# Performance work log

Measured on AMD Instinct MI355X. Metric: run time of the kernel, lower is better.

## Reference

```python
import jax, jax.numpy as jnp
import numpy as np
from jax import lax

EPS = 1e-5


def _up2_align_corners(x):
    # UpsamplingBilinear2d(scale_factor=2) => align_corners=True
    B, C, H, W = x.shape
    def idx(n):
        pos = jnp.arange(2 * n, dtype=jnp.float32) * ((n - 1) / (2 * n - 1))
        i0 = jnp.floor(pos).astype(jnp.int32)
        i1 = jnp.minimum(i0 + 1, n - 1)
        f = (pos - i0).astype(x.dtype)
        return i0, i1, f
    i0, i1, f = idx(H)
    x = x[:, :, i0, :] * (1 - f)[None, None, :, None] + x[:, :, i1, :] * f[None, None, :, None]
    j0, j1, g = idx(W)
    x = x[:, :, :, j0] * (1 - g) + x[:, :, :, j1] * g
    return x


def _forward(x, w_off, b_off, w_dcn, b_dcn, gamma, beta, run_mean, run_var):
    B, C, H, W = x.shape
    Cout = w_dcn.shape[0]
    # conv_offset: 27 = deform_groups*3*3*3 channels -> (o1, o2, mask)
    om = lax.conv_general_dilated(x, w_off, (1, 1), ((1, 1), (1, 1)),
                                  dimension_numbers=('NCHW', 'OIHW', 'NCHW'))
    om = om + b_off[None, :, None, None]
    o1, o2, m = om[:, :9], om[:, 9:18], om[:, 18:]
    off = jnp.concatenate([o1, o2], axis=1)          # [B,18,H,W]
    dy = off[:, 0::2]                                 # [B,9,H,W] per-kernel-point dy
    dx = off[:, 1::2]                                 # [B,9,H,W] per-kernel-point dx
    mask = jax.nn.sigmoid(m)                          # [B,9,H,W]
    # sampling positions: p + p_k + offset, stride=1, pad=1, dilation=1
    ky = jnp.array([-1, -1, -1, 0, 0, 0, 1, 1, 1], jnp.float32)
    kx = jnp.array([-1, 0, 1, -1, 0, 1, -1, 0, 1], jnp.float32)
    py = dy + jnp.arange(H, dtype=jnp.float32)[None, None, :, None] + ky[None, :, None, None]
    px = dx + jnp.arange(W, dtype=jnp.float32)[None, None, None, :] + kx[None, :, None, None]
    y0 = jnp.floor(py); x0 = jnp.floor(px)
    fy = py - y0; fx = px - x0
    y0i = y0.astype(jnp.int32); x0i = x0.astype(jnp.int32)
    xf = x.reshape(B, C, H * W)
    KHW = 9 * H * W
    def gather(yi, xi, wgt):
        valid = ((yi >= 0) & (yi < H) & (xi >= 0) & (xi < W)).astype(x.dtype)
        idx = jnp.clip(yi, 0, H - 1) * W + jnp.clip(xi, 0, W - 1)
        g = jnp.take_along_axis(xf, jnp.broadcast_to(idx.reshape(B, 1, KHW), (B, C, KHW)), axis=2)
        return g.reshape(B, C, 9, H, W) * (wgt * valid)[:, None]
    s = (gather(y0i, x0i, (1 - fy) * (1 - fx))
         + gather(y0i, x0i + 1, (1 - fy) * fx)
         + gather(y0i + 1, x0i, fy * (1 - fx))
         + gather(y0i + 1, x0i + 1, fy * fx))
    s = s * mask[:, None]                             # modulated sampling
    out = jnp.einsum('bckhw,ock->bohw', s, w_dcn.reshape(Cout, C, 9))
    out = out + b_dcn[None, :, None, None]
    # BatchNorm (eval mode with running stats) + ReLU
    scale = (gamma * lax.rsqrt(run_var + EPS))[None, :, None, None]
    out = out * scale + (beta - gamma * run_mean * lax.rsqrt(run_var + EPS))[None, :, None, None]
    out = jax.nn.relu(out)
    return _up2_align_corners(out)


def setup_inputs() -> dict:
    key = jax.random.key(0)
    ks = jax.random.split(key, 9)
    B, Cin, H, W, Cout = 4, 256, 64, 64, 128
    x = jax.random.normal(ks[0], (B, Cin, H, W), jnp.float32)
    w_off = jax.random.normal(ks[1], (27, Cin, 3, 3), jnp.float32) * 0.01
    b_off = jax.random.normal(ks[2], (27,), jnp.float32) * 0.1
    w_dcn = jax.random.normal(ks[3], (Cout, Cin, 3, 3), jnp.float32) * 0.05
    b_dcn = jax.random.normal(ks[4], (Cout,), jnp.float32) * 0.01
    gamma = 1.0 + 0.1 * jax.random.normal(ks[5], (Cout,), jnp.float32)
    beta = 0.1 * jax.random.normal(ks[6], (Cout,), jnp.float32)
    run_mean = 0.1 * jax.random.normal(ks[7], (Cout,), jnp.float32)
    run_var = jax.random.uniform(ks[8], (Cout,), jnp.float32) + 0.5
    return {"x": x, "w_off": w_off, "b_off": b_off, "w_dcn": w_dcn, "b_dcn": b_dcn,
            "gamma": gamma, "beta": beta, "run_mean": run_mean, "run_var": run_var}


def reference(x, w_off, b_off, w_dcn, b_dcn, gamma, beta, run_mean, run_var):
    return _forward(x, w_off, b_off, w_dcn, b_dcn, gamma, beta, run_mean, run_var)
```

## Files before the change

### kernel.cpp

```cpp
#include <hip/hip_runtime.h>
#include <math.h>

#define CIN  256
#define COUT 128
#define HW   4096
#define NB   4
#define OCSPLIT 4
#define CSPLIT  2
#define CPC  (CIN / CSPLIT)
#define SFLAV (576 * 16)

typedef short short8v __attribute__((ext_vector_type(8)));
typedef float f32x4  __attribute__((ext_vector_type(4)));

__global__ __launch_bounds__(256) void k_prep_w(
    const float* __restrict__ w_dcn, const float* __restrict__ b_dcn,
    const float* __restrict__ gamma, const float* __restrict__ beta,
    const float* __restrict__ rmean, const float* __restrict__ rvar,
    unsigned short* __restrict__ w_hi, unsigned short* __restrict__ w_lo,
    float* __restrict__ bias_t)
{
  int t = blockIdx.x * 256 + threadIdx.x;
  if (t < COUT) {
    float sc = gamma[t] * rsqrtf(rvar[t] + 1e-5f);
    bias_t[t] = b_dcn[t] * sc + beta[t] - rmean[t] * sc;
  }
  if (t >= CIN * COUT * 9) return;
  int k = t % 9;
  int q = t / 9;
  int co = q % COUT;
  int c  = q / COUT;
  float sc = gamma[co] * rsqrtf(rvar[co] + 1e-5f);
  float w = w_dcn[((size_t)co * CIN + c) * 9 + k] * sc;
  unsigned int wb = __float_as_uint(w);
  unsigned short hi = (unsigned short)(wb >> 16);
  float lof = w - __uint_as_float(wb & 0xFFFF0000u);
  unsigned short lo = (unsigned short)(__float_as_uint(lof) >> 16);
  size_t idx = (((size_t)k * 32 + (c >> 3)) * 128 + co) * 8 + (c & 7);
  w_hi[idx] = hi;
  w_lo[idx] = lo;
}

__global__ __launch_bounds__(256) void k_prep_wo(
    const float* __restrict__ w_off,
    unsigned short* __restrict__ wo_hi, unsigned short* __restrict__ wo_lo)
{
  int t = blockIdx.x * 256 + threadIdx.x;
  if (t >= 9 * 32 * 32 * 8) return;
  int ce = t & 7;
  int co = (t >> 3) & 31;
  int cq = (t >> 8) & 31;
  int k  = t >> 13;
  int c = cq * 8 + ce;
  float w = (co < 27) ? w_off[((size_t)co * CIN + c) * 9 + k] : 0.f;
  unsigned int wb = __float_as_uint(w);
  unsigned short hi = (unsigned short)(wb >> 16);
  float lof = w - __uint_as_float(wb & 0xFFFF0000u);
  unsigned short lo = (unsigned short)(__float_as_uint(lof) >> 16);
  wo_hi[t] = hi;
  wo_lo[t] = lo;
}

__global__ __launch_bounds__(256, 4) void k_off_mfma(
    const float* __restrict__ x,
    const unsigned short* __restrict__ wo_hi, const unsigned short* __restrict__ wo_lo,
    float* __restrict__ om_part)
{
  int blk = (blockIdx.x & 7) * 128 + (blockIdx.x >> 3);
  int split = blk & 3;
  int bh = blk >> 2;
  int b = bh >> 6, h = bh & 63;
  int t = threadIdx.x;
  int lane = t & 63;
  int wv = t >> 6;
  int lrow = lane & 15, lgrp = lane >> 4;

  __shared__ __align__(16) unsigned int win_hi[3 * 66 * 20];
  __shared__ __align__(16) unsigned int win_lo[3 * 66 * 20];

  f32x4 acc[2];
  acc[0] = (f32x4){0.f, 0.f, 0.f, 0.f};
  acc[1] = (f32x4){0.f, 0.f, 0.f, 0.f};

  const float* xb = x + (size_t)b * CIN * HW;

  for (int chunk = 0; chunk < 2; ++chunk) {
    int cbase = split * 64 + chunk * 32;
    for (int i = t; i < 3168; i += 256) {
      int cp = i / 198;
      int s  = i - cp * 198;
      int r  = s / 66;
      int colp = s - r * 66;
      int row = h + r - 1;
      int col = colp - 1;
      bool v = ((unsigned)row < 64u) && ((unsigned)col < 64u);
      int ch = cbase + 2 * cp;
      float f0 = 0.f, f1 = 0.f;
      if (v) {
        const float* xp = xb + ((size_t)ch * 64 + row) * 64 + col;
        f0 = xp[0];
        f1 = xp[HW];
      }
      unsigned a0 = __float_as_uint(f0), a1 = __float_as_uint(f1);
      unsigned hi = (a0 >> 16) | (a1 & 0xFFFF0000u);
      float l0 = f0 - __uint_as_float(a0 & 0xFFFF0000u);
      float l1 = f1 - __uint_as_float(a1 & 0xFFFF0000u);
      unsigned lo = (__float_as_uint(l0) >> 16) | (__float_as_uint(l1) & 0xFFFF0000u);
      win_hi[s * 20 + cp] = hi;
      win_lo[s * 20 + cp] = lo;
    }
    __syncthreads();

    int pos = wv * 16 + lrow;
#pragma unroll
    for (int k = 0; k < 9; ++k) {
      int ky = k / 3 - 1, kx = k % 3 - 1;
      int slot = (ky + 1) * 66 + pos + kx + 1;
      const unsigned int* ph = &win_hi[slot * 20 + lgrp * 4];
      const unsigned int* pl = &win_lo[slot * 20 + lgrp * 4];
      short8v bh = *(const short8v*)ph;
      short8v bl = *(const short8v*)pl;
#pragma unroll
      for (int m = 0; m < 2; ++m) {
        size_t widx = (((size_t)k * 32 + (cbase >> 3) + lgrp) * 32 + m * 16 + lrow) * 8;
        short8v ah = *(const short8v*)(wo_hi + widx);
        short8v al = *(const short8v*)(wo_lo + widx);
        acc[m] = __builtin_amdgcn_mfma_f32_16x16x32_bf16(ah, bh, acc[m], 0, 0, 0);
        acc[m] = __builtin_amdgcn_mfma_f32_16x16x32_bf16(ah, bl, acc[m], 0, 0, 0);
        acc[m] = __builtin_amdgcn_mfma_f32_16x16x32_bf16(al, bh, acc[m], 0, 0, 0);
      }
    }
    __syncthreads();
  }

  int pos = wv * 16 + lrow;
#pragma unroll
  for (int m = 0; m < 2; ++m)
#pragma unroll
    for (int j = 0; j < 4; ++j) {
      int co = m * 16 + lgrp * 4 + j;
      if (co < 27)
        om_part[(((size_t)split * NB + b) * 27 + co) * HW + h * 64 + pos] = acc[m][j];
    }
}

__global__ __launch_bounds__(256) void k_prep_md(
    const float* __restrict__ om_part, const float* __restrict__ b_off,
    float4* __restrict__ md_w, int4* __restrict__ md_i)
{
  int t = blockIdx.x * 256 + threadIdx.x;
  if (t >= NB * 9 * HW) return;
  int hw = t & 4095;
  int bk = t >> 12;
  int k = bk % 9;
  int b = bk / 9;
  int h = hw >> 6, w = hw & 63;

  float dy = b_off[2 * k], dx = b_off[2 * k + 1], mr = b_off[18 + k];
#pragma unroll
  for (int s = 0; s < OCSPLIT; ++s) {
    size_t o = ((size_t)s * NB + b) * 27 * HW + hw;
    dy += om_part[o + (size_t)(2 * k) * HW];
    dx += om_part[o + (size_t)(2 * k + 1) * HW];
    mr += om_part[o + (size_t)(18 + k) * HW];
  }
  float m = 1.0f / (1.0f + expf(-mr));

  int ky = k / 3 - 1, kx = k % 3 - 1;
  float py = dy + (float)h + (float)ky;
  float px = dx + (float)w + (float)kx;
  float y0f = floorf(py), x0f = floorf(px);
  float fy = py - y0f, fx = px - x0f;
  int y0 = (int)y0f, x0 = (int)x0f;
  int y1 = y0 + 1, x1 = x0 + 1;

  bool vy0 = (y0 >= 0) & (y0 < 64), vy1 = (y1 >= 0) & (y1 < 64);
  bool vx0 = (x0 >= 0) & (x0 < 64), vx1 = (x1 >= 0) & (x1 < 64);
  int cy0 = min(max(y0, 0), 63), cy1 = min(max(y1, 0), 63);
  int cx0 = min(max(x0, 0), 63), cx1 = min(max(x1, 0), 63);

  float4 wv;
  wv.x = (vy0 && vx0) ? (1.f - fy) * (1.f - fx) * m : 0.f;
  wv.y = (vy0 && vx1) ? (1.f - fy) * fx * m : 0.f;
  wv.z = (vy1 && vx0) ? fy * (1.f - fx) * m : 0.f;
  wv.w = (vy1 && vx1) ? fy * fx * m : 0.f;
  int4 iv;
  iv.x = cy0 * 64 + cx0;
  iv.y = cy0 * 64 + cx1;
  iv.z = cy1 * 64 + cx0;
  iv.w = cy1 * 64 + cx1;
  md_w[t] = wv;
  md_i[t] = iv;
}

__global__ __launch_bounds__(256, 3) void k_dcn(
    const float* __restrict__ x,
    const unsigned short* __restrict__ w_hi, const unsigned short* __restrict__ w_lo,
    const float4* __restrict__ md_w, const int4* __restrict__ md_i,
    float* __restrict__ part)
{
  int blk = (blockIdx.x & 7) * 64 + (blockIdx.x >> 3);
  int h = blk & 63;
  int b = (blk >> 6) & (NB - 1);
  int s2 = blk >> 8;
  int c0 = s2 * CPC;
  int t = threadIdx.x;
  int lane = t & 63;
  int wv = t >> 6;
  int lrow = lane & 15, lgrp = lane >> 4;

  __shared__ __align__(16) unsigned int sbuf[SFLAV];
  __shared__ __align__(16) float win[8 * 64 * 4];

  int W0 = min(max(h - 3, 0), 56);
  int ob = W0 * 64;

  int k0 = t >> 6;
  size_t mdbase = (size_t)b * 9 * HW;
  size_t mdp = mdbase + (size_t)h * 64 + (t & 63);
  float4 mw0 = md_w[mdp + (size_t)k0 * HW];
  int4  mi0 = md_i[mdp + (size_t)k0 * HW];
  float4 mw1 = md_w[mdp + (size_t)(k0 + 4) * HW];
  int4  mi1 = md_i[mdp + (size_t)(k0 + 4) * HW];
  bool hasC = (t < 64);
  float4 mw2 = make_float4(0.f, 0.f, 0.f, 0.f);
  int4  mi2 = make_int4(0, 0, 0, 0);
  if (hasC) {
    mw2 = md_w[mdp + (size_t)8 * HW];
    mi2 = md_i[mdp + (size_t)8 * HW];
  }
  int fast0 = __all(((unsigned)(mi0.x - ob) < 512u) && ((unsigned)(mi0.z - ob) < 512u));
  int fast1 = __all(((unsigned)(mi1.x - ob) < 512u) && ((unsigned)(mi1.z - ob) < 512u));
  int fast2 = __all(((unsigned)(mi2.x - ob) < 512u) && ((unsigned)(mi2.z - ob) < 512u));

  f32x4 acc[2][4];
#pragma unroll
  for (int m = 0; m < 2; ++m)
#pragma unroll
    for (int nt = 0; nt < 4; ++nt)
      acc[m][nt] = (f32x4){0.f, 0.f, 0.f, 0.f};

  const float* xb = x + (size_t)b * CIN * HW;

#define GATHER(MW, MI, FASTE, ROW)                                              \
  {                                                                             \
    float s0_, s1_, s2_, s3_;                                                   \
    if (FASTE) {                                                                \
      float4 T0 = *(const float4*)&win[(MI.x - ob) * 4];                        \
      float4 T1 = *(const float4*)&win[(MI.y - ob) * 4];                        \
      float4 T2 = *(const float4*)&win[(MI.z - ob) * 4];                        \
      float4 T3 = *(const float4*)&win[(MI.w - ob) * 4];                        \
      s0_ = MW.x * T0.x + MW.y * T1.x + MW.z * T2.x + MW.w * T3.x;              \
      s1_ = MW.x * T0.y + MW.y * T1.y + MW.z * T2.y + MW.w * T3.y;              \
      s2_ = MW.x * T0.z + MW.y * T1.z + MW.z * T2.z + MW.w * T3.z;              \
      s3_ = MW.x * T0.w + MW.y * T1.w + MW.z * T2.w + MW.w * T3.w;              \
    } else {                                                                    \
      const float* xc_ = xb + (size_t)c4 * HW;                                  \
      s0_ = MW.x * xc_[MI.x] + MW.y * xc_[MI.y] + MW.z * xc_[MI.z] + MW.w * xc_[MI.w]; \
      xc_ += HW;                                                                \
      s1_ = MW.x * xc_[MI.x] + MW.y * xc_[MI.y] + MW.z * xc_[MI.z] + MW.w * xc_[MI.w]; \
      xc_ += HW;                                                                \
      s2_ = MW.x * xc_[MI.x] + MW.y * xc_[MI.y] + MW.z * xc_[MI.z] + MW.w * xc_[MI.w]; \
      xc_ += HW;                                                                \
      s3_ = MW.x * xc_[MI.x] + MW.y * xc_[MI.y] + MW.z * xc_[MI.z] + MW.w * xc_[MI.w]; \
    }                                                                           \
    unsigned a0_ = __float_as_uint(s0_) + 0x8000u;                              \
    unsigned a1_ = __float_as_uint(s1_) + 0x8000u;                              \
    unsigned a2_ = __float_as_uint(s2_) + 0x8000u;                              \
    unsigned a3_ = __float_as_uint(s3_) + 0x8000u;                              \
    unsigned hiA_ = (a0_ >> 16) | (a1_ & 0xFFFF0000u);                          \
    unsigned hiB_ = (a2_ >> 16) | (a3_ & 0xFFFF0000u);                          \
    int cp0_ = 2 * step;                                                        \
    int quad_ = (((ROW) >> 2) + (cp0_ >> 2)) & 3;                               \
    int word_ = (ROW) * 16 + quad_ * 4 + (cp0_ & 3);                            \
    *(uint2*)&sbuf[word_] = make_uint2(hiA_, hiB_);                             \
  }

  for (int chunk = 0; chunk < CPC / 32; ++chunk) {
    int cbase = c0 + chunk * 32;
    for (int step = 0; step < 8; ++step) {
      int c4 = cbase + step * 4;
      {
        const float* xsb = xb + (size_t)(c4 + (t & 3)) * HW + ob + (t >> 2);
        int ldsbase = t & ~63;
#pragma unroll
        for (int j = 0; j < 8; ++j)
          __builtin_amdgcn_global_load_lds(
              (const __attribute__((address_space(1))) void*)(xsb + j * 64),
              (__attribute__((address_space(3))) void*)&win[j * 256 + ldsbase],
              4, 0, 0);
      }
      __syncthreads();
      GATHER(mw0, mi0, fast0, t)
      GATHER(mw1, mi1, fast1, 256 + t)
      if (hasC) GATHER(mw2, mi2, fast2, 512 + t)
      __syncthreads();
    }

    __builtin_amdgcn_s_setprio(1);
#pragma unroll
    for (int k = 0; k < 9; ++k) {
      short8v bh[4];
#pragma unroll
      for (int nt = 0; nt < 4; ++nt) {
        int row = k * 64 + nt * 16 + lrow;
        int quad = ((row >> 2) + lgrp) & 3;
        bh[nt] = *(const short8v*)&sbuf[row * 16 + quad * 4];
      }
#pragma unroll
      for (int m = 0; m < 2; ++m) {
        size_t widx = (((size_t)k * 32 + (cbase >> 3) + lgrp) * 128 + (wv * 32 + m * 16 + lrow)) * 8;
        short8v ah = *(const short8v*)(w_hi + widx);
        short8v al = *(const short8v*)(w_lo + widx);
#pragma unroll
        for (int nt = 0; nt < 4; ++nt) {
          acc[m][nt] = __builtin_amdgcn_mfma_f32_16x16x32_bf16(ah, bh[nt], acc[m][nt], 0, 0, 0);
          acc[m][nt] = __builtin_amdgcn_mfma_f32_16x16x32_bf16(al, bh[nt], acc[m][nt], 0, 0, 0);
        }
      }
    }
    __builtin_amdgcn_s_setprio(0);
    __syncthreads();
  }
#undef GATHER

#pragma unroll
  for (int m = 0; m < 2; ++m)
#pragma unroll
    for (int nt = 0; nt < 4; ++nt)
#pragma unroll
      for (int j = 0; j < 4; ++j) {
        int co = wv * 32 + m * 16 + lgrp * 4 + j;
        int p = h * 64 + nt * 16 + lrow;
        part[(((size_t)s2 * NB + b) * COUT + co) * HW + p] = acc[m][nt][j];
      }
}

__global__ __launch_bounds__(256) void k_upred(
    const float* __restrict__ part, const float* __restrict__ bias_t,
    float* __restrict__ out)
{
  int bid = (blockIdx.x & 7) * 4096 + (blockIdx.x >> 3);
  int t = bid * 256 + threadIdx.x;
  if (t >= NB * COUT * 128 * 128) return;
  int j = t & 127;
  int i = (t >> 7) & 127;
  int bc = t >> 14;
  int co = bc & (COUT - 1);
  const float R = (float)(63.0 / 127.0);
  float pi = (float)i * R;
  float pj = (float)j * R;
  float i0f = floorf(pi), j0f = floorf(pj);
  int i0 = (int)i0f, j0 = (int)j0f;
  int i1 = min(i0 + 1, 63), j1 = min(j0 + 1, 63);
  float f = pi - i0f, g = pj - j0f;
  const float* p0 = part + (size_t)bc * HW;
  const float* p1 = part + (size_t)(CSPLIT - 1) * NB * COUT * HW + (size_t)bc * HW;
  float bv = bias_t[co];
  float a  = fmaxf(p0[i0 * 64 + j0] + p1[i0 * 64 + j0] + bv, 0.f);
  float bb = fmaxf(p0[i0 * 64 + j1] + p1[i0 * 64 + j1] + bv, 0.f);
  float cc = fmaxf(p0[i1 * 64 + j0] + p1[i1 * 64 + j0] + bv, 0.f);
  float dd = fmaxf(p0[i1 * 64 + j1] + p1[i1 * 64 + j1] + bv, 0.f);
  float t0 = a * (1.f - f) + cc * f;
  float t1 = bb * (1.f - f) + dd * f;
  out[t] = t0 * (1.f - g) + t1 * g;
}

extern "C" void kernel_launch(void* const* d_in, const int* in_sizes, int n_in,
                              void* d_out, int out_size, void* d_ws, size_t ws_size,
                              hipStream_t stream)
{
  const float* x     = (const float*)d_in[0];
  const float* w_off = (const float*)d_in[1];
  const float* b_off = (const float*)d_in[2];
  const float* w_dcn = (const float*)d_in[3];
  const float* b_dcn = (const float*)d_in[4];
  const float* gamma = (const float*)d_in[5];
  const float* beta  = (const float*)d_in[6];
  const float* rmean = (const float*)d_in[7];
  const float* rvar  = (const float*)d_in[8];
  float* out = (float*)d_out;

  char* ws = (char*)d_ws;
  size_t off = 0;
  auto alloc = [&](size_t bytes) {
    void* p = ws + off;
    off = (off + bytes + 255) & ~255UL;
    return p;
  };
  float*  om_part = (float*) alloc(sizeof(float)  * OCSPLIT * NB * 27 * HW);
  float4* md_w    = (float4*)alloc(sizeof(float4) * NB * 9 * HW);
  int4*   md_i    = (int4*)  alloc(sizeof(int4)   * NB * 9 * HW);
  unsigned short* w_hi = (unsigned short*)alloc(sizeof(unsigned short) * 9 * CIN * COUT);
  unsigned short* w_lo = (unsigned short*)alloc(sizeof(unsigned short) * 9 * CIN * COUT);
  unsigned short* wo_hi = (unsigned short*)alloc(sizeof(unsigned short) * 9 * 32 * 32 * 8);
  unsigned short* wo_lo = (unsigned short*)alloc(sizeof(unsigned short) * 9 * 32 * 32 * 8);
  float*  bias_t  = (float*) alloc(sizeof(float)  * COUT);
  float*  part    = (float*) alloc(sizeof(float)  * CSPLIT * NB * COUT * HW);
  (void)ws_size; (void)in_sizes; (void)n_in; (void)out_size;

  k_prep_w<<<(CIN * COUT * 9 + 255) / 256, 256, 0, stream>>>(
      w_dcn, b_dcn, gamma, beta, rmean, rvar, w_hi, w_lo, bias_t);
  k_prep_wo<<<(9 * 32 * 32 * 8 + 255) / 256, 256, 0, stream>>>(w_off, wo_hi, wo_lo);
  k_off_mfma<<<NB * 64 * 4, 256, 0, stream>>>(x, wo_hi, wo_lo, om_part);
  k_prep_md<<<(NB * 9 * HW + 255) / 256, 256, 0, stream>>>(om_part, b_off, md_w, md_i);
  k_dcn<<<CSPLIT * NB * 64, 256, 0, stream>>>(x, w_hi, w_lo, md_w, md_i, part);
  k_upred<<<(NB * COUT * 128 * 128 + 255) / 256, 256, 0, stream>>>(part, bias_t, out);
}
```

Measured before the change: 105.1 us.

## Double-buffer the LDS input window to overlap global loads with gathering

New measurement: 115.9 us. +10.3%, slower.

```diff
diff --git a/kernel.cpp b/kernel.cpp
--- a/kernel.cpp
+++ b/kernel.cpp
@@ -210,7 +210,7 @@
   int lrow = lane & 15, lgrp = lane >> 4;
 
   __shared__ __align__(16) unsigned int sbuf[SFLAV];
-  __shared__ __align__(16) float win[8 * 64 * 4];
+  __shared__ __align__(16) float win[2 * 2048];
 
   int W0 = min(max(h - 3, 0), 56);
   int ob = W0 * 64;
@@ -241,15 +241,28 @@
       acc[m][nt] = (f32x4){0.f, 0.f, 0.f, 0.f};
 
   const float* xb = x + (size_t)b * CIN * HW;
+  int ldsbase = t & ~63;
+
+#define ISSUE_STAGE(CSTART, BUF)                                                \
+  {                                                                             \
+    const float* xsb_ = xb + (size_t)((CSTART) + (t & 3)) * HW + ob + (t >> 2); \
+    float* wdst_ = &win[(BUF) * 2048 + ldsbase];                                \
+    _Pragma("unroll")                                                           \
+    for (int j_ = 0; j_ < 8; ++j_)                                              \
+      __builtin_amdgcn_global_load_lds(                                         \
+          (const __attribute__((address_space(1))) void*)(xsb_ + j_ * 64),      \
+          (__attribute__((address_space(3))) void*)(wdst_ + j_ * 256),          \
+          4, 0, 0);                                                             \
+  }
 
 #define GATHER(MW, MI, FASTE, ROW)                                              \
   {                                                                             \
     float s0_, s1_, s2_, s3_;                                                   \
     if (FASTE) {                                                                \
-      float4 T0 = *(const float4*)&win[(MI.x - ob) * 4];                        \
-      float4 T1 = *(const float4*)&win[(MI.y - ob) * 4];                        \
-      float4 T2 = *(const float4*)&win[(MI.z - ob) * 4];                        \
-      float4 T3 = *(const float4*)&win[(MI.w - ob) * 4];                        \
+      float4 T0 = *(const float4*)&wcur[(MI.x - ob) * 4];                       \
+      float4 T1 = *(const float4*)&wcur[(MI.y - ob) * 4];                       \
+      float4 T2 = *(const float4*)&wcur[(MI.z - ob) * 4];                       \
+      float4 T3 = *(const float4*)&wcur[(MI.w - ob) * 4];                       \
       s0_ = MW.x * T0.x + MW.y * T1.x + MW.z * T2.x + MW.w * T3.x;              \
       s1_ = MW.x * T0.y + MW.y * T1.y + MW.z * T2.y + MW.w * T3.y;              \
       s2_ = MW.x * T0.z + MW.y * T1.z + MW.z * T2.z + MW.w * T3.z;              \
@@ -276,21 +289,20 @@
     *(uint2*)&sbuf[word_] = make_uint2(hiA_, hiB_);                             \
   }
 
-  for (int chunk = 0; chunk < CPC / 32; ++chunk) {
+  ISSUE_STAGE(c0, 0)
+  __syncthreads();
+
+  const int NCHUNK = CPC / 32;
+  for (int chunk = 0; chunk < NCHUNK; ++chunk) {
     int cbase = c0 + chunk * 32;
     for (int step = 0; step < 8; ++step) {
       int c4 = cbase + step * 4;
-      {
-        const float* xsb = xb + (size_t)(c4 + (t & 3)) * HW + ob + (t >> 2);
-        int ldsbase = t & ~63;
-#pragma unroll
-        for (int j = 0; j < 8; ++j)
-          __builtin_amdgcn_global_load_lds(
-              (const __attribute__((address_space(1))) void*)(xsb + j * 64),
-              (__attribute__((address_space(3))) void*)&win[j * 256 + ldsbase],
-              4, 0, 0);
-      }
-      __syncthreads();
+      if (step < 7) {
+        ISSUE_STAGE(cbase + (step + 1) * 4, (step + 1) & 1)
+      } else if (chunk + 1 < NCHUNK) {
+        ISSUE_STAGE(c0 + (chunk + 1) * 32, 0)
+      }
+      const float* wcur = &win[(step & 1) * 2048];
       GATHER(mw0, mi0, fast0, t)
       GATHER(mw1, mi1, fast1, 256 + t)
       if (hasC) GATHER(mw2, mi2, fast2, 512 + t)
@@ -323,6 +335,7 @@
     __syncthreads();
   }
 #undef GATHER
+#undef ISSUE_STAGE
 
 #pragma unroll
   for (int m = 0; m < 2; ++m)
```
